# Kernel optimization log

Hardware: AMD Instinct MI355X
Metric: run time of the kernel (lower is better)

## Reference

```python
import jax, jax.numpy as jnp
import numpy as np


def setup_inputs() -> dict:
    key = jax.random.key(0)
    k_x, k_b = jax.random.split(key)
    B, C, H, W = 32, 512, 32, 32
    x = jax.random.normal(k_x, (B, C, H, W), dtype=jnp.float32)
    beta = jax.random.normal(k_b, (1,), dtype=jnp.float32)
    return {"x": x, "beta": beta}


def reference(x, beta):
    B, C, H, W = x.shape
    feat = x.reshape(B, C, H * W)                       # [B, C, N]
    # channel-channel Gram matrix: [B, C, C]
    attn = jnp.einsum('bcn,bdn->bcd', feat, feat)
    # DANet-style reversed scores: rowmax - score, then softmax over last dim
    attn = jnp.max(attn, axis=-1, keepdims=True) - attn
    attn = jax.nn.softmax(attn, axis=-1)
    feat_e = jnp.einsum('bcd,bdn->bcn', attn, feat).reshape(B, C, H, W)
    return beta * feat_e + x
```

## Files before the change

### kernel.cpp

```cpp
#include <hip/hip_runtime.h>
#include <math.h>

constexpr int B = 32, C = 512, N = 1024;

typedef float f32x4 __attribute__((ext_vector_type(4)));
typedef short s16x8 __attribute__((ext_vector_type(8)));
typedef unsigned short u16x4 __attribute__((ext_vector_type(4)));

__device__ __forceinline__ unsigned short f32_to_bf16(float v) {
  union { float f; unsigned u; } a; a.f = v;
  unsigned r = (a.u + 0x7FFFu + ((a.u >> 16) & 1u)) >> 16;
  return (unsigned short)r;
}
__device__ __forceinline__ float bf16_to_f32(unsigned short h) {
  union { float f; unsigned u; } a; a.u = ((unsigned)h) << 16;
  return a.f;
}

__device__ __forceinline__ void glds16(const void* g, void* l) {
  __builtin_amdgcn_global_load_lds((const __attribute__((address_space(1))) void*)g,
                                   (__attribute__((address_space(3))) void*)l, 16, 0, 0);
}

__global__ __launch_bounds__(256) void convert_kernel(const float* __restrict__ x,
                                                      unsigned short* __restrict__ xh,
                                                      unsigned short* __restrict__ xl,
                                                      unsigned short* __restrict__ xhT) {
  const int b = blockIdx.z;
  const int cy = blockIdx.y * 64;
  const int nx = blockIdx.x * 64;
  const int t = threadIdx.x;
  const int r = t >> 4, c4 = (t & 15) * 4;

  __shared__ unsigned short T[64][68];

#pragma unroll
  for (int rr = 0; rr < 64; rr += 16) {
    const int row = rr + r;
    const size_t gi = ((size_t)b * C + cy + row) * N + nx + c4;
    const float4 v = *(const float4*)&x[gi];
    u16x4 h, l;
    h[0] = f32_to_bf16(v.x); l[0] = f32_to_bf16(v.x - bf16_to_f32(h[0]));
    h[1] = f32_to_bf16(v.y); l[1] = f32_to_bf16(v.y - bf16_to_f32(h[1]));
    h[2] = f32_to_bf16(v.z); l[2] = f32_to_bf16(v.z - bf16_to_f32(h[2]));
    h[3] = f32_to_bf16(v.w); l[3] = f32_to_bf16(v.w - bf16_to_f32(h[3]));
    *(u16x4*)&xh[gi] = h;
    *(u16x4*)&xl[gi] = l;
    T[row][c4 + 0] = h[0]; T[row][c4 + 1] = h[1];
    T[row][c4 + 2] = h[2]; T[row][c4 + 3] = h[3];
  }
  __syncthreads();
#pragma unroll
  for (int rr = 0; rr < 64; rr += 16) {
    const int nrow = rr + r;
    u16x4 o;
    o[0] = T[c4 + 0][nrow]; o[1] = T[c4 + 1][nrow];
    o[2] = T[c4 + 2][nrow]; o[3] = T[c4 + 3][nrow];
    *(u16x4*)&xhT[((size_t)b * N + nx + nrow) * C + cy + c4] = o;
  }
}

__global__ __launch_bounds__(512, 4) void gram_mfma(const unsigned short* __restrict__ xh,
                                                    const unsigned short* __restrict__ xl,
                                                    float* __restrict__ G) {
  const int l = blockIdx.x;
  const int xcd = l & 7, seq = l >> 3;
  const int b = xcd + 8 * (seq >> 4);
  const int tile = seq & 15;
  const int i0 = (tile >> 2) * 128, j0 = (tile & 3) * 128;

  const unsigned short* __restrict__ Fh = xh + (size_t)b * C * N;
  const unsigned short* __restrict__ Fl = xl + (size_t)b * C * N;
  float* __restrict__ Gb = G + (size_t)b * C * C;

  __shared__ __align__(16) unsigned short Ah[128 * 64], Al[128 * 64],
                                          Bh[128 * 64], Bl[128 * 64];

  const int t = threadIdx.x, wave = t >> 6, lane = t & 63;
  const int wi = wave >> 1, wj = wave & 1;
  const int lrow = lane & 15, quad = lane >> 4;
  const int srow8 = lane >> 3;
  const int sel = ((lane & 7) ^ srow8) * 8;

  f32x4 acc[2][4] = {};

  for (int k0 = 0; k0 < N; k0 += 64) {
    __syncthreads();
#pragma unroll
    for (int cc = 0; cc < 2; ++cc) {
      const int chunk = wave * 2 + cc;
      const int row = chunk * 8 + srow8;
      const size_t gA = (size_t)(i0 + row) * N + k0 + sel;
      const size_t gB = (size_t)(j0 + row) * N + k0 + sel;
      glds16(Fh + gA, &Ah[chunk * 512]);
      glds16(Fl + gA, &Al[chunk * 512]);
      glds16(Fh + gB, &Bh[chunk * 512]);
      glds16(Fl + gB, &Bl[chunk * 512]);
    }
    __syncthreads();

#pragma unroll
    for (int kh = 0; kh < 2; ++kh) {
      s16x8 ah[2], al[2], bh[4], bl[4];
#pragma unroll
      for (int ti = 0; ti < 2; ++ti) {
        const int r = wi * 32 + ti * 16 + lrow;
        const int off = r * 64 + ((kh * 4 + quad) ^ (r & 7)) * 8;
        ah[ti] = *(const s16x8*)&Ah[off];
        al[ti] = *(const s16x8*)&Al[off];
      }
#pragma unroll
      for (int tj = 0; tj < 4; ++tj) {
        const int r = wj * 64 + tj * 16 + lrow;
        const int off = r * 64 + ((kh * 4 + quad) ^ (r & 7)) * 8;
        bh[tj] = *(const s16x8*)&Bh[off];
        bl[tj] = *(const s16x8*)&Bl[off];
      }
#pragma unroll
      for (int ti = 0; ti < 2; ++ti)
#pragma unroll
        for (int tj = 0; tj < 4; ++tj) {
          acc[ti][tj] = __builtin_amdgcn_mfma_f32_16x16x32_bf16(ah[ti], bh[tj], acc[ti][tj], 0, 0, 0);
          acc[ti][tj] = __builtin_amdgcn_mfma_f32_16x16x32_bf16(ah[ti], bl[tj], acc[ti][tj], 0, 0, 0);
          acc[ti][tj] = __builtin_amdgcn_mfma_f32_16x16x32_bf16(al[ti], bh[tj], acc[ti][tj], 0, 0, 0);
        }
    }
  }

#pragma unroll
  for (int ti = 0; ti < 2; ++ti) {
    const int gr0 = i0 + wi * 32 + ti * 16 + quad * 4;
#pragma unroll
    for (int tj = 0; tj < 4; ++tj) {
      const int gc = j0 + wj * 64 + tj * 16 + lrow;
#pragma unroll
      for (int r = 0; r < 4; ++r)
        Gb[(size_t)(gr0 + r) * C + gc] = acc[ti][tj][r];
    }
  }
}

__global__ __launch_bounds__(256) void softmax_kernel(const float* __restrict__ G,
                                                      unsigned short* __restrict__ A) {
  const int t = threadIdx.x;
  const int r = t >> 7;
  const int c = t & 127;
  const size_t row = (size_t)blockIdx.x * 2 + r;

  const float4 v = *(const float4*)&G[row * C + c * 4];
  float mn = fminf(fminf(v.x, v.y), fminf(v.z, v.w));
#pragma unroll
  for (int o = 32; o > 0; o >>= 1) mn = fminf(mn, __shfl_xor(mn, o, 64));

  __shared__ float redmin[4], redsum[4];
  const int w = t >> 6;
  if ((t & 63) == 0) redmin[w] = mn;
  __syncthreads();
  mn = fminf(redmin[r * 2], redmin[r * 2 + 1]);

  const float e0 = __expf(mn - v.x), e1 = __expf(mn - v.y);
  const float e2 = __expf(mn - v.z), e3 = __expf(mn - v.w);
  float s = e0 + e1 + e2 + e3;
#pragma unroll
  for (int o = 32; o > 0; o >>= 1) s += __shfl_xor(s, o, 64);
  if ((t & 63) == 0) redsum[w] = s;
  __syncthreads();
  s = redsum[r * 2] + redsum[r * 2 + 1];

  const float inv = 1.0f / s;
  u16x4 o4;
  o4[0] = f32_to_bf16(e0 * inv); o4[1] = f32_to_bf16(e1 * inv);
  o4[2] = f32_to_bf16(e2 * inv); o4[3] = f32_to_bf16(e3 * inv);
  *(u16x4*)&A[row * C + c * 4] = o4;
}

__global__ __launch_bounds__(256, 4) void av_mfma(const unsigned short* __restrict__ Abf,
                                                  const unsigned short* __restrict__ xhT,
                                                  const float* __restrict__ x,
                                                  const float* __restrict__ beta,
                                                  float* __restrict__ out) {
  const int l = blockIdx.x;
  const int xcd = l & 7, seq = l >> 3;
  const int b = xcd + 8 * (seq >> 5);
  const int tile = seq & 31;
  const int i0 = (tile >> 3) * 128;
  const int j0 = (tile & 7) * 128;

  const unsigned short* __restrict__ Ab = Abf + (size_t)b * C * C;
  const unsigned short* __restrict__ FT = xhT + (size_t)b * N * C;
  const float* __restrict__ xb = x + (size_t)b * C * N;
  float* __restrict__ ob = out + (size_t)b * C * N;

  __shared__ __align__(16) unsigned short SMEM[2 * 128 * 64];
  unsigned short* As = SMEM;
  unsigned short* Bs = SMEM + 128 * 64;

  const int t = threadIdx.x, wave = t >> 6, lane = t & 63;
  const int wi = wave >> 1, wj = wave & 1;
  const int lrow = lane & 15, quad = lane >> 4;
  const int srow8 = lane >> 3;
  const int sel = ((lane & 7) ^ srow8) * 8;

  f32x4 acc[4][4] = {};

  for (int k0 = 0; k0 < C; k0 += 64) {
    __syncthreads();
#pragma unroll
    for (int cc = 0; cc < 4; ++cc) {
      const int chunk = wave * 4 + cc;
      const int row = chunk * 8 + srow8;
      glds16(Ab + (size_t)(i0 + row) * C + k0 + sel, &As[chunk * 512]);
      glds16(FT + (size_t)(j0 + row) * C + k0 + sel, &Bs[chunk * 512]);
    }
    __syncthreads();

#pragma unroll
    for (int kh = 0; kh < 2; ++kh) {
      s16x8 af[4], bf[4];
#pragma unroll
      for (int ti = 0; ti < 4; ++ti) {
        const int r = wi * 64 + ti * 16 + lrow;
        af[ti] = *(const s16x8*)&As[r * 64 + ((kh * 4 + quad) ^ (r & 7)) * 8];
      }
#pragma unroll
      for (int tj = 0; tj < 4; ++tj) {
        const int r = wj * 64 + tj * 16 + lrow;
        bf[tj] = *(const s16x8*)&Bs[r * 64 + ((kh * 4 + quad) ^ (r & 7)) * 8];
      }
#pragma unroll
      for (int ti = 0; ti < 4; ++ti)
#pragma unroll
        for (int tj = 0; tj < 4; ++tj)
          acc[ti][tj] = __builtin_amdgcn_mfma_f32_16x16x32_bf16(af[ti], bf[tj], acc[ti][tj], 0, 0, 0);
    }
  }

  __syncthreads();
  float* fs = (float*)SMEM + wave * 1024;
  const float bv = beta[0];
#pragma unroll
  for (int ti = 0; ti < 4; ++ti) {
#pragma unroll
    for (int tj = 0; tj < 4; ++tj)
#pragma unroll
      for (int r = 0; r < 4; ++r)
        fs[(quad * 4 + r) * 64 + tj * 16 + lrow] = acc[ti][tj][r];
    __syncthreads();
#pragma unroll
    for (int p = 0; p < 4; ++p) {
      const int f = p * 64 + lane;
      const int rr = f >> 4, cc4 = (f & 15) * 4;
      const f32x4 e = *(const f32x4*)&fs[rr * 64 + cc4];
      const int gr = i0 + wi * 64 + ti * 16 + rr;
      const int gc = j0 + wj * 64 + cc4;
      const size_t o = (size_t)gr * N + gc;
      const float4 xv = *(const float4*)&xb[o];
      float4 ov;
      ov.x = fmaf(bv, e[0], xv.x);
      ov.y = fmaf(bv, e[1], xv.y);
      ov.z = fmaf(bv, e[2], xv.z);
      ov.w = fmaf(bv, e[3], xv.w);
      *(float4*)&ob[o] = ov;
    }
    __syncthreads();
  }
}

extern "C" void kernel_launch(void* const* d_in, const int* in_sizes, int n_in,
                              void* d_out, int out_size, void* d_ws, size_t ws_size,
                              hipStream_t stream) {
  const float* x    = (const float*)d_in[0];
  const float* beta = (const float*)d_in[1];
  float* out = (float*)d_out;

  char* ws = (char*)d_ws;
  float* G            = (float*)ws;          ws += (size_t)B * C * C * 4;
  unsigned short* xh  = (unsigned short*)ws; ws += (size_t)B * C * N * 2;
  unsigned short* xl  = (unsigned short*)ws; ws += (size_t)B * C * N * 2;
  unsigned short* xhT = (unsigned short*)ws; ws += (size_t)B * N * C * 2;
  unsigned short* Abf = (unsigned short*)ws;

  convert_kernel<<<dim3(N / 64, C / 64, B), dim3(256), 0, stream>>>(x, xh, xl, xhT);
  gram_mfma     <<<dim3(512),               dim3(512), 0, stream>>>(xh, xl, G);
  softmax_kernel<<<dim3(B * C / 2),         dim3(256), 0, stream>>>(G, Abf);
  av_mfma       <<<dim3(1024),              dim3(256), 0, stream>>>(Abf, xhT, x, beta, out);
}
```

Before: 205.2 us.

## Fuse Gram matrix computation with reversed softmax in one kernel

```diff
diff --git a/kernel.cpp b/kernel.cpp
--- a/kernel.cpp
+++ b/kernel.cpp
@@ -60,118 +60,141 @@
   }
 }
 
-__global__ __launch_bounds__(512, 4) void gram_mfma(const unsigned short* __restrict__ xh,
+__global__ __launch_bounds__(512, 2) void gram_soft(const unsigned short* __restrict__ xh,
                                                     const unsigned short* __restrict__ xl,
-                                                    float* __restrict__ G) {
+                                                    unsigned short* __restrict__ Abf) {
   const int l = blockIdx.x;
   const int xcd = l & 7, seq = l >> 3;
-  const int b = xcd + 8 * (seq >> 4);
-  const int tile = seq & 15;
-  const int i0 = (tile >> 2) * 128, j0 = (tile & 3) * 128;
+  const int b = xcd + 8 * (seq >> 3);
+  const int i0 = (seq & 7) * 64;
 
   const unsigned short* __restrict__ Fh = xh + (size_t)b * C * N;
   const unsigned short* __restrict__ Fl = xl + (size_t)b * C * N;
-  float* __restrict__ Gb = G + (size_t)b * C * C;
-
-  __shared__ __align__(16) unsigned short Ah[128 * 64], Al[128 * 64],
-                                          Bh[128 * 64], Bl[128 * 64];
+  unsigned short* __restrict__ Ab = Abf + (size_t)b * C * C;
+
+  __shared__ __align__(16) unsigned short Bh[512 * 32];
+  __shared__ __align__(16) unsigned short Bl[512 * 32];
 
   const int t = threadIdx.x, wave = t >> 6, lane = t & 63;
-  const int wi = wave >> 1, wj = wave & 1;
   const int lrow = lane & 15, quad = lane >> 4;
-  const int srow8 = lane >> 3;
-  const int sel = ((lane & 7) ^ srow8) * 8;
-
-  f32x4 acc[2][4] = {};
-
-  for (int k0 = 0; k0 < N; k0 += 64) {
-    __syncthreads();
-#pragma unroll
-    for (int cc = 0; cc < 2; ++cc) {
-      const int chunk = wave * 2 + cc;
-      const int row = chunk * 8 + srow8;
-      const size_t gA = (size_t)(i0 + row) * N + k0 + sel;
-      const size_t gB = (size_t)(j0 + row) * N + k0 + sel;
-      glds16(Fh + gA, &Ah[chunk * 512]);
-      glds16(Fl + gA, &Al[chunk * 512]);
-      glds16(Fh + gB, &Bh[chunk * 512]);
-      glds16(Fl + gB, &Bl[chunk * 512]);
-    }
-    __syncthreads();
-
-#pragma unroll
-    for (int kh = 0; kh < 2; ++kh) {
-      s16x8 ah[2], al[2], bh[4], bl[4];
-#pragma unroll
-      for (int ti = 0; ti < 2; ++ti) {
-        const int r = wi * 32 + ti * 16 + lrow;
-        const int off = r * 64 + ((kh * 4 + quad) ^ (r & 7)) * 8;
-        ah[ti] = *(const s16x8*)&Ah[off];
-        al[ti] = *(const s16x8*)&Al[off];
-      }
+  const int srow = lane >> 2;
+  const int sel  = ((lane & 3) ^ (srow & 3)) * 8;
+
+  f32x4 acc[4][4] = {};
+
+  for (int k0 = 0; k0 < N; k0 += 32) {
+    __syncthreads();
+#pragma unroll
+    for (int cc = 0; cc < 4; ++cc) {
+      const int chunk = wave * 4 + cc;
+      const int row = chunk * 16 + srow;
+      const size_t g = (size_t)row * N + k0 + sel;
+      glds16(Fh + g, &Bh[chunk * 512]);
+      glds16(Fl + g, &Bl[chunk * 512]);
+    }
+    __syncthreads();
+
+    s16x8 ah[4], al[4], bh[4], bl[4];
+#pragma unroll
+    for (int ti = 0; ti < 4; ++ti) {
+      const int r = i0 + ti * 16 + lrow;
+      const int off = r * 32 + (quad ^ (r & 3)) * 8;
+      ah[ti] = *(const s16x8*)&Bh[off];
+      al[ti] = *(const s16x8*)&Bl[off];
+    }
+#pragma unroll
+    for (int tj = 0; tj < 4; ++tj) {
+      const int r = wave * 64 + tj * 16 + lrow;
+      const int off = r * 32 + (quad ^ (r & 3)) * 8;
+      bh[tj] = *(const s16x8*)&Bh[off];
+      bl[tj] = *(const s16x8*)&Bl[off];
+    }
+#pragma unroll
+    for (int ti = 0; ti < 4; ++ti)
 #pragma unroll
       for (int tj = 0; tj < 4; ++tj) {
-        const int r = wj * 64 + tj * 16 + lrow;
-        const int off = r * 64 + ((kh * 4 + quad) ^ (r & 7)) * 8;
-        bh[tj] = *(const s16x8*)&Bh[off];
-        bl[tj] = *(const s16x8*)&Bl[off];
-      }
-#pragma unroll
-      for (int ti = 0; ti < 2; ++ti)
-#pragma unroll
-        for (int tj = 0; tj < 4; ++tj) {
-          acc[ti][tj] = __builtin_amdgcn_mfma_f32_16x16x32_bf16(ah[ti], bh[tj], acc[ti][tj], 0, 0, 0);
-          acc[ti][tj] = __builtin_amdgcn_mfma_f32_16x16x32_bf16(ah[ti], bl[tj], acc[ti][tj], 0, 0, 0);
-          acc[ti][tj] = __builtin_amdgcn_mfma_f32_16x16x32_bf16(al[ti], bh[tj], acc[ti][tj], 0, 0, 0);
-        }
-    }
-  }
-
-#pragma unroll
-  for (int ti = 0; ti < 2; ++ti) {
-    const int gr0 = i0 + wi * 32 + ti * 16 + quad * 4;
-#pragma unroll
-    for (int tj = 0; tj < 4; ++tj) {
-      const int gc = j0 + wj * 64 + tj * 16 + lrow;
+        acc[ti][tj] = __builtin_amdgcn_mfma_f32_16x16x32_bf16(ah[ti], bh[tj], acc[ti][tj], 0, 0, 0);
+        acc[ti][tj] = __builtin_amdgcn_mfma_f32_16x16x32_bf16(ah[ti], bl[tj], acc[ti][tj], 0, 0, 0);
+        acc[ti][tj] = __builtin_amdgcn_mfma_f32_16x16x32_bf16(al[ti], bh[tj], acc[ti][tj], 0, 0, 0);
+      }
+  }
+
+  __syncthreads();
+  float* red = (float*)Bh;
+  float* fin = (float*)Bl;
+
+  float m[16];
+#pragma unroll
+  for (int ti = 0; ti < 4; ++ti)
+#pragma unroll
+    for (int r = 0; r < 4; ++r)
+      m[ti * 4 + r] = fminf(fminf(acc[ti][0][r], acc[ti][1][r]),
+                            fminf(acc[ti][2][r], acc[ti][3][r]));
+#pragma unroll
+  for (int o = 1; o < 16; o <<= 1)
+#pragma unroll
+    for (int s = 0; s < 16; ++s) m[s] = fminf(m[s], __shfl_xor(m[s], o, 64));
+  if (lrow == 0)
+#pragma unroll
+    for (int ti = 0; ti < 4; ++ti)
 #pragma unroll
       for (int r = 0; r < 4; ++r)
-        Gb[(size_t)(gr0 + r) * C + gc] = acc[ti][tj][r];
-    }
-  }
-}
-
-__global__ __launch_bounds__(256) void softmax_kernel(const float* __restrict__ G,
-                                                      unsigned short* __restrict__ A) {
-  const int t = threadIdx.x;
-  const int r = t >> 7;
-  const int c = t & 127;
-  const size_t row = (size_t)blockIdx.x * 2 + r;
-
-  const float4 v = *(const float4*)&G[row * C + c * 4];
-  float mn = fminf(fminf(v.x, v.y), fminf(v.z, v.w));
-#pragma unroll
-  for (int o = 32; o > 0; o >>= 1) mn = fminf(mn, __shfl_xor(mn, o, 64));
-
-  __shared__ float redmin[4], redsum[4];
-  const int w = t >> 6;
-  if ((t & 63) == 0) redmin[w] = mn;
-  __syncthreads();
-  mn = fminf(redmin[r * 2], redmin[r * 2 + 1]);
-
-  const float e0 = __expf(mn - v.x), e1 = __expf(mn - v.y);
-  const float e2 = __expf(mn - v.z), e3 = __expf(mn - v.w);
-  float s = e0 + e1 + e2 + e3;
-#pragma unroll
-  for (int o = 32; o > 0; o >>= 1) s += __shfl_xor(s, o, 64);
-  if ((t & 63) == 0) redsum[w] = s;
-  __syncthreads();
-  s = redsum[r * 2] + redsum[r * 2 + 1];
-
-  const float inv = 1.0f / s;
-  u16x4 o4;
-  o4[0] = f32_to_bf16(e0 * inv); o4[1] = f32_to_bf16(e1 * inv);
-  o4[2] = f32_to_bf16(e2 * inv); o4[3] = f32_to_bf16(e3 * inv);
-  *(u16x4*)&A[row * C + c * 4] = o4;
+        red[wave * 64 + ti * 16 + quad * 4 + r] = m[ti * 4 + r];
+  __syncthreads();
+  if (t < 64) {
+    float v = red[t];
+#pragma unroll
+    for (int w = 1; w < 8; ++w) v = fminf(v, red[w * 64 + t]);
+    fin[t] = v;
+  }
+  __syncthreads();
+
+  float sm[16];
+#pragma unroll
+  for (int ti = 0; ti < 4; ++ti)
+#pragma unroll
+    for (int r = 0; r < 4; ++r) {
+      const float mn = fin[ti * 16 + quad * 4 + r];
+      float s = 0.f;
+#pragma unroll
+      for (int tj = 0; tj < 4; ++tj) {
+        const float e = __expf(mn - acc[ti][tj][r]);
+        acc[ti][tj][r] = e;
+        s += e;
+      }
+      sm[ti * 4 + r] = s;
+    }
+#pragma unroll
+  for (int o = 1; o < 16; o <<= 1)
+#pragma unroll
+    for (int s = 0; s < 16; ++s) sm[s] += __shfl_xor(sm[s], o, 64);
+  if (lrow == 0)
+#pragma unroll
+    for (int ti = 0; ti < 4; ++ti)
+#pragma unroll
+      for (int r = 0; r < 4; ++r)
+        red[wave * 64 + ti * 16 + quad * 4 + r] = sm[ti * 4 + r];
+  __syncthreads();
+  if (t < 64) {
+    float v = 0.f;
+#pragma unroll
+    for (int w = 0; w < 8; ++w) v += red[w * 64 + t];
+    fin[t] = 1.0f / v;
+  }
+  __syncthreads();
+
+#pragma unroll
+  for (int ti = 0; ti < 4; ++ti)
+#pragma unroll
+    for (int r = 0; r < 4; ++r) {
+      const float inv = fin[ti * 16 + quad * 4 + r];
+      const int grow = i0 + ti * 16 + quad * 4 + r;
+#pragma unroll
+      for (int tj = 0; tj < 4; ++tj) {
+        const int gcol = wave * 64 + tj * 16 + lrow;
+        Ab[(size_t)grow * C + gcol] = f32_to_bf16(acc[ti][tj][r] * inv);
+      }
+    }
 }
 
 __global__ __launch_bounds__(256, 4) void av_mfma(const unsigned short* __restrict__ Abf,
@@ -274,14 +297,12 @@
   float* out = (float*)d_out;
 
   char* ws = (char*)d_ws;
-  float* G            = (float*)ws;          ws += (size_t)B * C * C * 4;
   unsigned short* xh  = (unsigned short*)ws; ws += (size_t)B * C * N * 2;
   unsigned short* xl  = (unsigned short*)ws; ws += (size_t)B * C * N * 2;
   unsigned short* xhT = (unsigned short*)ws; ws += (size_t)B * N * C * 2;
   unsigned short* Abf = (unsigned short*)ws;
 
   convert_kernel<<<dim3(N / 64, C / 64, B), dim3(256), 0, stream>>>(x, xh, xl, xhT);
-  gram_mfma     <<<dim3(512),               dim3(512), 0, stream>>>(xh, xl, G);
-  softmax_kernel<<<dim3(B * C / 2),         dim3(256), 0, stream>>>(G, Abf);
+  gram_soft     <<<dim3(256),               dim3(512), 0, stream>>>(xh, xl, Abf);
   av_mfma       <<<dim3(1024),              dim3(256), 0, stream>>>(Abf, xhT, x, beta, out);
 }
```

Measured after the change: 235.4 us. +14.7%, slower.
